# Optimization experiments

Measured on AMD Instinct MI355X. Metric: run time of the kernel, lower is better.

## Reference

```python
import jax, jax.numpy as jnp
import numpy as np

K = 7        # kernel_size
OUT = 10     # out_channels
CIN = 1      # in_channels
IH = 306     # input spatial size (square)
POOL = 10    # max_pool1d kernel/stride


def setup_inputs() -> dict:
    key = jax.random.key(0)
    k1, k2, k3 = jax.random.split(key, 3)
    stdv = 1.0 / np.sqrt(CIN * K * K)  # matches reset_parameters()
    x = jax.random.normal(k1, (1, CIN, IH, IH), dtype=jnp.float32)
    K_hit = jax.random.uniform(k2, (OUT, CIN, K, K), dtype=jnp.float32, minval=-stdv, maxval=stdv)
    K_miss = jax.random.uniform(k3, (OUT, CIN, K, K), dtype=jnp.float32, minval=-stdv, maxval=stdv)
    return {"input": x, "K_hit": K_hit, "K_miss": K_miss}


def _patches(x, k):
    # Sliding windows, stride 1, valid padding: (B, C, k, k, fh, fw).
    B, C, H, W = x.shape
    fh, fw = H - k + 1, W - k + 1
    rows = []
    for u in range(k):          # fixed small loop over kernel rows
        cols = [x[:, :, u:u + fh, v:v + fw] for v in range(k)]
        rows.append(jnp.stack(cols, axis=2))   # (B, C, k, fh, fw)
    return jnp.stack(rows, axis=2)             # (B, C, k, k, fh, fw)


def reference(input, K_hit, K_miss):
    B, cin, ih, _ = input.shape
    out, k = K_hit.shape[0], K_hit.shape[2]
    fh = ih - k + 1
    out_fmap = cin * out

    p = _patches(input, k)                                # (B, cin, k, k, fh, fh)
    p = p[:, None]                                        # (B, 1, cin, k, k, fh, fh)
    kh = K_hit[None, :, :, :, :, None, None]              # (1, out, cin, k, k, 1, 1)
    km = K_miss[None, :, :, :, :, None, None]

    # -relu(-(x - K_hit)) == min(x - K_hit, 0); summed over ALL windows + kernel taps -> (B, out)
    F_hit_sum = jnp.sum(jnp.minimum(p - kh, 0.0), axis=(2, 3, 4, 5, 6))
    F_miss_sum = jnp.sum(jnp.maximum(p - km, 0.0), axis=(2, 3, 4, 5, 6))
    F_map_val = F_hit_sum - F_miss_sum                    # (B, out)

    def expand(v):  # broadcast (B, out) scalar-per-channel over (cin*fh*fh), view as feature map
        return jnp.broadcast_to(v[:, :, None], (B, out, cin * fh * fh)).reshape(B, out_fmap, fh, fh)

    F_map = expand(F_map_val)
    F_hit_list = expand(F_hit_sum)
    F_miss_list = expand(F_miss_sum)

    # torch.squeeze then F.max_pool1d(kernel=10): pool over the last spatial axis.
    sq = jnp.squeeze(F_map)                               # (out_fmap, fh, fh) since B=1
    L = sq.shape[-1]
    nwin = L // POOL
    pooled = sq[..., : nwin * POOL].reshape(sq.shape[:-1] + (nwin, POOL)).max(-1)

    return pooled, F_hit_list, F_miss_list
```

## Files before the change

kernel.cpp:

```cpp
#include <hip/hip_runtime.h>

#define IHH 306
#define KW 7
#define OUTC 10
#define FH 300
#define NPIX (FH * FH)
#define KK (KW * KW)
#define BLK 256
#define NBA ((NPIX + BLK - 1) / BLK)
#define NROWS 21
#define OUT_TOTAL 1890000
#define POOLED_END 90000
#define HIT_END 990000


__global__ __launch_bounds__(BLK) void k_partials(
    const float* __restrict__ x,
    const float* __restrict__ kh,
    const float* __restrict__ km,
    float* __restrict__ partials,
    float* __restrict__ ksums)
{
    __shared__ float2 s_k[KK * OUTC];
    for (int t = threadIdx.x; t < KK * OUTC; t += BLK) {
        const int tap = t / OUTC;
        const int o = t - tap * OUTC;
        s_k[t] = make_float2(kh[o * KK + tap], km[o * KK + tap]);
    }
    __syncthreads();

    float ah[OUTC], am[OUTC];
    float sx = 0.0f;
#pragma unroll
    for (int o = 0; o < OUTC; ++o) { ah[o] = 0.0f; am[o] = 0.0f; }

    const int p = blockIdx.x * BLK + threadIdx.x;
    if (p < NPIX) {
        const int i = p / FH;
        const int j = p - i * FH;
        const float* xr = x + i * IHH + j;
        for (int u = 0; u < KW; ++u) {
            for (int v = 0; v < KW; ++v) {
                const float xv = xr[u * IHH + v];
                sx += xv;
                const float2* wk = &s_k[(u * KW + v) * OUTC];
#pragma unroll
                for (int o = 0; o < OUTC; ++o) {
                    const float2 w = wk[o];
                    ah[o] += fabsf(xv - w.x);
                    am[o] += fabsf(xv - w.y);
                }
            }
        }
    }

    const int lane = threadIdx.x & 63;
    const int wave = threadIdx.x >> 6;
    __shared__ float s_red[BLK / 64][NROWS];

    float vals[NROWS];
#pragma unroll
    for (int o = 0; o < OUTC; ++o) { vals[o] = ah[o]; vals[OUTC + o] = am[o]; }
    vals[2 * OUTC] = sx;

#pragma unroll
    for (int r = 0; r < NROWS; ++r) {
        float v = vals[r];
#pragma unroll
        for (int s = 32; s > 0; s >>= 1) v += __shfl_xor(v, s);
        if (lane == 0) s_red[wave][r] = v;
    }
    __syncthreads();
    if (threadIdx.x < NROWS) {
        const float s = s_red[0][threadIdx.x] + s_red[1][threadIdx.x]
                      + s_red[2][threadIdx.x] + s_red[3][threadIdx.x];
        partials[threadIdx.x * NBA + blockIdx.x] = s;
    }

    if (blockIdx.x == 0 && threadIdx.x < 2 * OUTC) {
        const float* kp = (threadIdx.x < OUTC)
            ? (kh + threadIdx.x * KK)
            : (km + (threadIdx.x - OUTC) * KK);
        float s = 0.0f;
        for (int t = 0; t < KK; ++t) s += kp[t];
        ksums[threadIdx.x] = s;
    }
}

__global__ __launch_bounds__(BLK) void k_fill(
    const float* __restrict__ partials,
    const float* __restrict__ ksums,
    float4* __restrict__ out)
{
    __shared__ float s_part[NROWS][8];
    __shared__ float s_o[3][OUTC];
    const int t = threadIdx.x;

    if (t < NROWS * 8) {
        const int r = t >> 3;
        const int s = t & 7;
        const float* row = partials + r * NBA;
        float acc = 0.0f;
        for (int c = s; c < NBA; c += 8) acc += row[c];
        s_part[r][s] = acc;
    }
    __syncthreads();
    if (t < NROWS) {
        float f = 0.0f;
#pragma unroll
        for (int s = 0; s < 8; ++s) f += s_part[t][s];
        s_part[t][0] = f;
    }
    __syncthreads();
    if (t < OUTC) {
        const float Sx = s_part[2 * OUTC][0];
        const float Ah = s_part[t][0];
        const float Am = s_part[OUTC + t][0];
        const float Fh = 0.5f * ((Sx - (float)NPIX * ksums[t]) - Ah);
        const float Fm = 0.5f * ((Sx - (float)NPIX * ksums[OUTC + t]) + Am);
        s_o[0][t] = Fh - Fm;
        s_o[1][t] = Fh;
        s_o[2][t] = Fm;
    }
    __syncthreads();

    const int idx4 = blockIdx.x * BLK + t;
    if (idx4 >= OUT_TOTAL / 4) return;
    const int base = idx4 * 4;
    float val;
    if (base < POOLED_END) {
        val = s_o[0][base / 9000];
    } else if (base < HIT_END) {
        val = s_o[1][(base - POOLED_END) / 90000];
    } else {
        val = s_o[2][(base - HIT_END) / 90000];
    }
    out[idx4] = make_float4(val, val, val, val);
}

extern "C" void kernel_launch(void* const* d_in, const int* in_sizes, int n_in,
                              void* d_out, int out_size, void* d_ws, size_t ws_size,
                              hipStream_t stream) {
    const float* x  = (const float*)d_in[0];
    const float* kh = (const float*)d_in[1];
    const float* km = (const float*)d_in[2];
    float* out = (float*)d_out;

    float* partials = (float*)d_ws;
    float* ksums    = partials + NROWS * NBA;

    k_partials<<<NBA, BLK, 0, stream>>>(x, kh, km, partials, ksums);

    const int n4 = OUT_TOTAL / 4;
    k_fill<<<(n4 + BLK - 1) / BLK, BLK, 0, stream>>>(partials, ksums, (float4*)out);
}
```

Measured before the change: 30.86 us.

## Fuse partial reduction and output fill into one kernel with a grid barrier

```diff
diff --git a/kernel.cpp b/kernel.cpp
--- a/kernel.cpp
+++ b/kernel.cpp
@@ -7,19 +7,41 @@
 #define NPIX (FH * FH)
 #define KK (KW * KW)
 #define BLK 256
-#define NBA ((NPIX + BLK - 1) / BLK)
+#define GRID 352
 #define NROWS 21
-#define OUT_TOTAL 1890000
+#define OUT4 472500
 #define POOLED_END 90000
 #define HIT_END 990000
+#define CHUNK4 1343
 
 
-__global__ __launch_bounds__(BLK) void k_partials(
+__device__ __forceinline__ void grid_barrier(int* cnt, int* flag) {
+    __syncthreads();
+    if (threadIdx.x == 0) {
+        __threadfence();
+        const int old = __hip_atomic_fetch_add(cnt, 1, __ATOMIC_ACQ_REL,
+                                               __HIP_MEMORY_SCOPE_AGENT);
+        if (old == GRID - 1) {
+            __hip_atomic_store(flag, 1, __ATOMIC_RELEASE,
+                               __HIP_MEMORY_SCOPE_AGENT);
+        } else {
+            while (__hip_atomic_load(flag, __ATOMIC_ACQUIRE,
+                                     __HIP_MEMORY_SCOPE_AGENT) == 0) {
+                __builtin_amdgcn_s_sleep(1);
+            }
+        }
+        __threadfence();
+    }
+    __syncthreads();
+}
+
+__global__ __launch_bounds__(BLK, 2) void k_fused(
     const float* __restrict__ x,
     const float* __restrict__ kh,
     const float* __restrict__ km,
     float* __restrict__ partials,
-    float* __restrict__ ksums)
+    int* __restrict__ bar,
+    float4* __restrict__ out)
 {
     __shared__ float2 s_k[KK * OUTC];
     for (int t = threadIdx.x; t < KK * OUTC; t += BLK) {
@@ -74,35 +96,29 @@
     if (threadIdx.x < NROWS) {
         const float s = s_red[0][threadIdx.x] + s_red[1][threadIdx.x]
                       + s_red[2][threadIdx.x] + s_red[3][threadIdx.x];
-        partials[threadIdx.x * NBA + blockIdx.x] = s;
+        partials[threadIdx.x * GRID + blockIdx.x] = s;
     }
 
-    if (blockIdx.x == 0 && threadIdx.x < 2 * OUTC) {
-        const float* kp = (threadIdx.x < OUTC)
-            ? (kh + threadIdx.x * KK)
-            : (km + (threadIdx.x - OUTC) * KK);
-        float s = 0.0f;
-        for (int t = 0; t < KK; ++t) s += kp[t];
-        ksums[threadIdx.x] = s;
-    }
-}
+    grid_barrier(&bar[0], &bar[1]);
 
-__global__ __launch_bounds__(BLK) void k_fill(
-    const float* __restrict__ partials,
-    const float* __restrict__ ksums,
-    float4* __restrict__ out)
-{
     __shared__ float s_part[NROWS][8];
+    __shared__ float s_ks[2 * OUTC];
     __shared__ float s_o[3][OUTC];
     const int t = threadIdx.x;
 
     if (t < NROWS * 8) {
         const int r = t >> 3;
-        const int s = t & 7;
-        const float* row = partials + r * NBA;
+        const int s8 = t & 7;
+        const float* row = partials + r * GRID;
         float acc = 0.0f;
-        for (int c = s; c < NBA; c += 8) acc += row[c];
-        s_part[r][s] = acc;
+        for (int c = s8; c < GRID; c += 8) acc += row[c];
+        s_part[r][s8] = acc;
+    } else if (t >= 192 && t < 192 + 2 * OUTC) {
+        const int a = t - 192;
+        const float* kp = (a < OUTC) ? (kh + a * KK) : (km + (a - OUTC) * KK);
+        float s = 0.0f;
+        for (int q = 0; q < KK; ++q) s += kp[q];
+        s_ks[a] = s;
     }
     __syncthreads();
     if (t < NROWS) {
@@ -116,26 +132,28 @@
         const float Sx = s_part[2 * OUTC][0];
         const float Ah = s_part[t][0];
         const float Am = s_part[OUTC + t][0];
-        const float Fh = 0.5f * ((Sx - (float)NPIX * ksums[t]) - Ah);
-        const float Fm = 0.5f * ((Sx - (float)NPIX * ksums[OUTC + t]) + Am);
+        const float Fh = 0.5f * ((Sx - (float)NPIX * s_ks[t]) - Ah);
+        const float Fm = 0.5f * ((Sx - (float)NPIX * s_ks[OUTC + t]) + Am);
         s_o[0][t] = Fh - Fm;
         s_o[1][t] = Fh;
         s_o[2][t] = Fm;
     }
     __syncthreads();
 
-    const int idx4 = blockIdx.x * BLK + t;
-    if (idx4 >= OUT_TOTAL / 4) return;
-    const int base = idx4 * 4;
-    float val;
-    if (base < POOLED_END) {
-        val = s_o[0][base / 9000];
-    } else if (base < HIT_END) {
-        val = s_o[1][(base - POOLED_END) / 90000];
-    } else {
-        val = s_o[2][(base - HIT_END) / 90000];
+    const int start = blockIdx.x * CHUNK4;
+    const int stop = min(start + CHUNK4, OUT4);
+    for (int i4 = start + t; i4 < stop; i4 += BLK) {
+        const int base = i4 * 4;
+        float v;
+        if (base < POOLED_END) {
+            v = s_o[0][base / 9000];
+        } else if (base < HIT_END) {
+            v = s_o[1][(base - POOLED_END) / 90000];
+        } else {
+            v = s_o[2][(base - HIT_END) / 90000];
+        }
+        out[i4] = make_float4(v, v, v, v);
     }
-    out[idx4] = make_float4(val, val, val, val);
 }
 
 extern "C" void kernel_launch(void* const* d_in, const int* in_sizes, int n_in,
@@ -144,13 +162,11 @@
     const float* x  = (const float*)d_in[0];
     const float* kh = (const float*)d_in[1];
     const float* km = (const float*)d_in[2];
-    float* out = (float*)d_out;
+    float4* out = (float4*)d_out;
 
     float* partials = (float*)d_ws;
-    float* ksums    = partials + NROWS * NBA;
+    int* bar = (int*)((char*)d_ws + 32768);
 
-    k_partials<<<NBA, BLK, 0, stream>>>(x, kh, km, partials, ksums);
-
-    const int n4 = OUT_TOTAL / 4;
-    k_fill<<<(n4 + BLK - 1) / BLK, BLK, 0, stream>>>(partials, ksums, (float4*)out);
+    (void)hipMemsetAsync(bar, 0, 128, stream);
+    k_fused<<<GRID, BLK, 0, stream>>>(x, kh, km, partials, bar, out);
 }
```

Result: slower. 71.25 us (+130.9%).

## Load kernel weights as uniform scalars and size the grid to one block per CU

Applied to the files above, without the earlier changes.

```diff
diff --git a/kernel.cpp b/kernel.cpp
--- a/kernel.cpp
+++ b/kernel.cpp
@@ -7,7 +7,8 @@
 #define NPIX (FH * FH)
 #define KK (KW * KW)
 #define BLK 256
-#define NBA ((NPIX + BLK - 1) / BLK)
+#define PPB 352
+#define NBP 256
 #define NROWS 21
 #define OUT_TOTAL 1890000
 #define POOLED_END 90000
@@ -21,34 +22,36 @@
     float* __restrict__ partials,
     float* __restrict__ ksums)
 {
-    __shared__ float2 s_k[KK * OUTC];
-    for (int t = threadIdx.x; t < KK * OUTC; t += BLK) {
-        const int tap = t / OUTC;
-        const int o = t - tap * OUTC;
-        s_k[t] = make_float2(kh[o * KK + tap], km[o * KK + tap]);
-    }
-    __syncthreads();
-
     float ah[OUTC], am[OUTC];
     float sx = 0.0f;
 #pragma unroll
     for (int o = 0; o < OUTC; ++o) { ah[o] = 0.0f; am[o] = 0.0f; }
 
-    const int p = blockIdx.x * BLK + threadIdx.x;
-    if (p < NPIX) {
-        const int i = p / FH;
-        const int j = p - i * FH;
-        const float* xr = x + i * IHH + j;
-        for (int u = 0; u < KW; ++u) {
-            for (int v = 0; v < KW; ++v) {
-                const float xv = xr[u * IHH + v];
-                sx += xv;
-                const float2* wk = &s_k[(u * KW + v) * OUTC];
+    const int base = blockIdx.x * PPB;
+#pragma unroll 1
+    for (int it = 0; it < 2; ++it) {
+        const int off = it * BLK + threadIdx.x;
+        const int p = base + off;
+        if (off < PPB && p < NPIX) {
+            const int i = p / FH;
+            const int j = p - i * FH;
+            const float* xr = x + i * IHH + j;
+#pragma unroll 1
+            for (int u = 0; u < KW; ++u) {
+                float xv[KW];
+#pragma unroll
+                for (int v = 0; v < KW; ++v) xv[v] = xr[u * IHH + v];
+#pragma unroll
+                for (int v = 0; v < KW; ++v) sx += xv[v];
+                const float* khu = kh + u * KW;
+                const float* kmu = km + u * KW;
 #pragma unroll
                 for (int o = 0; o < OUTC; ++o) {
-                    const float2 w = wk[o];
-                    ah[o] += fabsf(xv - w.x);
-                    am[o] += fabsf(xv - w.y);
+#pragma unroll
+                    for (int v = 0; v < KW; ++v) {
+                        ah[o] += fabsf(xv[v] - khu[o * KK + v]);
+                        am[o] += fabsf(xv[v] - kmu[o * KK + v]);
+                    }
                 }
             }
         }
@@ -74,7 +77,7 @@
     if (threadIdx.x < NROWS) {
         const float s = s_red[0][threadIdx.x] + s_red[1][threadIdx.x]
                       + s_red[2][threadIdx.x] + s_red[3][threadIdx.x];
-        partials[threadIdx.x * NBA + blockIdx.x] = s;
+        partials[threadIdx.x * NBP + blockIdx.x] = s;
     }
 
     if (blockIdx.x == 0 && threadIdx.x < 2 * OUTC) {
@@ -99,9 +102,9 @@
     if (t < NROWS * 8) {
         const int r = t >> 3;
         const int s = t & 7;
-        const float* row = partials + r * NBA;
+        const float* row = partials + r * NBP;
         float acc = 0.0f;
-        for (int c = s; c < NBA; c += 8) acc += row[c];
+        for (int c = s; c < NBP; c += 8) acc += row[c];
         s_part[r][s] = acc;
     }
     __syncthreads();
@@ -147,9 +150,9 @@
     float* out = (float*)d_out;
 
     float* partials = (float*)d_ws;
-    float* ksums    = partials + NROWS * NBA;
+    float* ksums    = partials + NROWS * NBP;
 
-    k_partials<<<NBA, BLK, 0, stream>>>(x, kh, km, partials, ksums);
+    k_partials<<<NBP, BLK, 0, stream>>>(x, kh, km, partials, ksums);
 
     const int n4 = OUT_TOTAL / 4;
     k_fill<<<(n4 + BLK - 1) / BLK, BLK, 0, stream>>>(partials, ksums, (float4*)out);
```

Measured after the change: 33.15 us. 1.07x slower.
